# Optimization experiments

Measured on AMD Instinct MI355X. Metric: run time of the kernel, lower is better.

Reference implementation:

```python
import jax, jax.numpy as jnp
import numpy as np

N, E, NFEAT, H = 100000, 1600000, 128, 128
NLAYER = 3


def setup_inputs() -> dict:
    key = jax.random.key(0)
    ks = jax.random.split(key, 20)
    s = 0.05
    return {
        "features": jax.random.normal(ks[0], (N, NFEAT), jnp.float32),
        "edge_index": jax.random.randint(ks[1], (2, E), 0, N, jnp.int32),
        "edge_weight": jax.random.uniform(ks[2], (E,), jnp.float32),
        "w1": jax.random.normal(ks[3], (H, NFEAT), jnp.float32) * s,
        "b1": jnp.zeros((H,), jnp.float32),
        "gin_w1": jax.random.normal(ks[4], (NLAYER, H, H), jnp.float32) * s,
        "gin_b1": jnp.zeros((NLAYER, H), jnp.float32),
        "gin_w2": jax.random.normal(ks[5], (NLAYER, H, H), jnp.float32) * s,
        "gin_b2": jnp.zeros((NLAYER, H), jnp.float32),
        "gru_wih": jax.random.normal(ks[6], (NLAYER, 3 * H, H), jnp.float32) * s,
        "gru_whh": jax.random.normal(ks[7], (NLAYER, 3 * H, H), jnp.float32) * s,
        "gru_bih": jnp.zeros((NLAYER, 3 * H), jnp.float32),
        "gru_bhh": jnp.zeros((NLAYER, 3 * H), jnp.float32),
        "head_w1": jax.random.normal(ks[8], (NLAYER, H, H), jnp.float32) * s,
        "head_b1": jnp.zeros((NLAYER, H), jnp.float32),
        "head_w2_0": jax.random.normal(ks[9], (2, H), jnp.float32) * s,
        "head_b2_0": jnp.zeros((2,), jnp.float32),
        "head_w2_1": jax.random.normal(ks[10], (6, H), jnp.float32) * s,
        "head_b2_1": jnp.zeros((6,), jnp.float32),
        "head_w2_2": jax.random.normal(ks[11], (21, H), jnp.float32) * s,
        "head_b2_2": jnp.zeros((21,), jnp.float32),
    }


def _gru_cell(x, h, wih, whh, bih, bhh):
    # torch.nn.GRUCell semantics
    gi = x @ wih.T + bih           # [N, 3H]
    gh = h @ whh.T + bhh           # [N, 3H]
    ir, iz, inn = jnp.split(gi, 3, axis=1)
    hr, hz, hn = jnp.split(gh, 3, axis=1)
    r = jax.nn.sigmoid(ir + hr)
    z = jax.nn.sigmoid(iz + hz)
    n = jnp.tanh(inn + r * hn)
    return (1.0 - z) * n + z * h


def reference(features, edge_index, edge_weight, w1, b1,
              gin_w1, gin_b1, gin_w2, gin_b2,
              gru_wih, gru_whh, gru_bih, gru_bhh,
              head_w1, head_b1,
              head_w2_0, head_b2_0, head_w2_1, head_b2_1, head_w2_2, head_b2_2):
    n_nodes = features.shape[0]
    dst, src = edge_index[0], edge_index[1]  # spmm: out[dst] += w * x[src]
    head_w2 = [head_w2_0, head_w2_1, head_w2_2]
    head_b2 = [head_b2_0, head_b2_1, head_b2_2]

    x = jax.nn.relu(features @ w1.T + b1)  # mlp1 + ReLU
    layer_info = x
    outputs, _outputs = [], []
    for i in range(NLAYER):
        agg = jax.ops.segment_sum(edge_weight[:, None] * x[src], dst,
                                  num_segments=n_nodes)
        h = _gru_cell(agg, layer_info, gru_wih[i], gru_whh[i],
                      gru_bih[i], gru_bhh[i])
        # GinMlp: Linear -> ReLU -> Linear, then outer ReLU
        x = jax.nn.relu(h @ gin_w1[i].T + gin_b1[i]) @ gin_w2[i].T + gin_b2[i]
        x = jax.nn.relu(x)
        # custom layer-norm variant
        x = x / jnp.sqrt(1.0 + jnp.sum(x * x, axis=1, keepdims=True))
        # prediction head for this layer (mlpPos = [0,1,2])
        tmp = jax.nn.relu(x @ head_w1[i].T + head_b1[i]) @ head_w2[i].T + head_b2[i]
        outputs.append(jax.nn.log_softmax(tmp, axis=1))
        _outputs.append(jax.nn.softmax(tmp, axis=1))
        layer_info = x
    return tuple(outputs) + tuple(_outputs)
```

## Files before the change

### kernel.cpp

```cpp
#include <hip/hip_runtime.h>
#include <cstdint>
#include <cstddef>


typedef short  v8s __attribute__((ext_vector_type(8)));
typedef float  v4f __attribute__((ext_vector_type(4)));

static __device__ __forceinline__ float bf2f(uint16_t u) {
  return __uint_as_float(((uint32_t)u) << 16);
}
static __device__ __forceinline__ uint16_t f2b(float f) {
  uint32_t x = __float_as_uint(f);
  return (uint16_t)((x + 0x7FFFu + ((x >> 16) & 1u)) >> 16);
}
static __device__ __forceinline__ float sigmoidf_(float v) {
  return 1.f / (1.f + __expf(-v));
}

__global__ void k_detect(const uint32_t* __restrict__ u, int* __restrict__ flag) {
  int lane = threadIdx.x;
  uint32_t low = u[lane] & 0xFFFFu;
  uint32_t e = (low >> 7) & 0xFFu;
  bool pass = (e == 0) || (e >= 110 && e <= 141);
  unsigned long long b = __ballot(pass);
  if (lane == 0) *flag = (__popcll(b) >= 32) ? 1 : 0;
}

struct CvtDesc {
  const void* src[18];
  int off[19];
};

__global__ void k_cvtw(CvtDesc c, float* __restrict__ wbase,
                       uint16_t* __restrict__ wb16,
                       const int* __restrict__ flag, int total) {
  int gid = blockIdx.x * 256 + threadIdx.x;
  if (gid >= total) return;
  int t = 0;
#pragma unroll
  for (int i = 1; i < 18; i++)
    if (gid >= c.off[i]) t = i;
  int local = gid - c.off[t];
  float v;
  if (*flag) v = bf2f(((const uint16_t*)c.src[t])[local]);
  else       v = ((const float*)c.src[t])[local];
  wbase[gid] = v;
  wb16[gid] = f2b(v);
}

__global__ void k_cvt_feat(const void* __restrict__ src, uint16_t* __restrict__ dst,
                           int n, const int* __restrict__ flag) {
  int i = blockIdx.x * 256 + threadIdx.x;
  if (i >= n) return;
  if (*flag) dst[i] = ((const uint16_t*)src)[i];
  else       dst[i] = f2b(((const float*)src)[i]);
}

__global__ void k_zero_i(int* __restrict__ p, int n) {
  int i = blockIdx.x * 256 + threadIdx.x;
  if (i < n) p[i] = 0;
}

__global__ void k_zero_f(float* __restrict__ p, int n) {
  int i = blockIdx.x * 256 + threadIdx.x;
  if (i < n) p[i] = 0.f;
}

__global__ void k_pack_mm(const uint16_t* __restrict__ src, uint16_t* __restrict__ dst,
                          int nmat) {
  int id = blockIdx.x * 256 + threadIdx.x;
  if (id >= nmat * 2048) return;
  int mat = id >> 11;
  int rem = id & 2047;
  int blk = rem >> 6, lane = rem & 63;
  int kc = blk >> 3, t = blk & 7;
  int n0 = lane & 15, quad = lane >> 4;
  const uint16_t* s = src + (size_t)mat * 16384 + (size_t)(t * 16 + n0) * 128 + kc * 32 + quad * 8;
  uint16_t* d = dst + (size_t)id * 8;
  *reinterpret_cast<v8s*>(d) = *reinterpret_cast<const v8s*>(s);
}

__global__ void k_pack_gru(const uint16_t* __restrict__ wih, const uint16_t* __restrict__ whh,
                           uint16_t* __restrict__ dst, int nlayer) {
  int id = blockIdx.x * 256 + threadIdx.x;
  if (id >= nlayer * 192 * 64) return;
  int lane = id & 63;
  int blk = (id >> 6) % 192;
  int layer = (id >> 6) / 192;
  int g = blk % 3;
  int mat = (blk / 3) % 2;
  int u = (blk / 6) % 2;
  int w = (blk / 12) % 4;
  int kc = blk / 48;
  int n0 = lane & 15, quad = lane >> 4;
  const uint16_t* base = (mat == 0 ? wih : whh) + (size_t)layer * 384 * 128;
  const uint16_t* s = base + (size_t)(g * 128 + w * 32 + u * 16 + n0) * 128 + kc * 32 + quad * 8;
  uint16_t* d = dst + ((size_t)layer * 192 + blk) * 512 + (size_t)lane * 8;
  *reinterpret_cast<v8s*>(d) = *reinterpret_cast<const v8s*>(s);
}

__global__ void k_hist(const int* __restrict__ dst, int* __restrict__ deg2, int E) {
  int e = blockIdx.x * 256 + threadIdx.x;
  if (e < E) atomicAdd(&deg2[(size_t)dst[e] * 8 + (blockIdx.x & 7)], 1);
}

__global__ void k_scan1(const int* __restrict__ deg, int* __restrict__ bsum, int n) {
  __shared__ int red[256];
  int t = threadIdx.x;
  int base = blockIdx.x * 1024;
  int s = 0;
#pragma unroll
  for (int i = 0; i < 4; i++) {
    int idx = base + i * 256 + t;
    if (idx < n) s += deg[idx];
  }
  red[t] = s;
  __syncthreads();
  for (int off = 128; off > 0; off >>= 1) {
    if (t < off) red[t] += red[t + off];
    __syncthreads();
  }
  if (t == 0) bsum[blockIdx.x] = red[0];
}

__global__ void k_scan2(int* bsum, int nb, int* rowptr, int n) {
  __shared__ int red[256];
  int t = threadIdx.x;
  int v[4];
  int s = 0;
#pragma unroll
  for (int i = 0; i < 4; i++) {
    int idx = t * 4 + i;
    v[i] = (idx < nb) ? bsum[idx] : 0;
    s += v[i];
  }
  red[t] = s;
  __syncthreads();
  for (int off = 1; off < 256; off <<= 1) {
    int u = (t >= off) ? red[t - off] : 0;
    __syncthreads();
    red[t] += u;
    __syncthreads();
  }
  int run = red[t] - s;
#pragma unroll
  for (int i = 0; i < 4; i++) {
    int idx = t * 4 + i;
    if (idx < nb) { bsum[idx] = run; run += v[i]; }
  }
  if (t == 255) rowptr[n] = red[255];
}

__global__ void k_scan3(const int* __restrict__ deg, const int* __restrict__ bsum,
                        int* __restrict__ rowptr, int* __restrict__ cursor, int n) {
  __shared__ int lds[256];
  int t = threadIdx.x;
  int base = blockIdx.x * 1024 + t * 4;
  int v0 = 0, v1 = 0, v2 = 0, v3 = 0;
  if (base + 0 < n) v0 = deg[base + 0];
  if (base + 1 < n) v1 = deg[base + 1];
  if (base + 2 < n) v2 = deg[base + 2];
  if (base + 3 < n) v3 = deg[base + 3];
  int s = v0 + v1 + v2 + v3;
  lds[t] = s;
  __syncthreads();
  for (int off = 1; off < 256; off <<= 1) {
    int u = (t >= off) ? lds[t - off] : 0;
    __syncthreads();
    lds[t] += u;
    __syncthreads();
  }
  int run = lds[t] - s + bsum[blockIdx.x];
  if (base + 0 < n) { rowptr[base + 0] = run; cursor[base + 0] = run; run += v0; }
  if (base + 1 < n) { rowptr[base + 1] = run; cursor[base + 1] = run; run += v1; }
  if (base + 2 < n) { rowptr[base + 2] = run; cursor[base + 2] = run; run += v2; }
  if (base + 3 < n) { rowptr[base + 3] = run; cursor[base + 3] = run; run += v3; }
}

__global__ void k_scatter(const int* __restrict__ dst, const int* __restrict__ src,
                          const void* __restrict__ w, int* __restrict__ cursor2,
                          uint2* __restrict__ ep, const int* __restrict__ flag, int E) {
  int e = blockIdx.x * 256 + threadIdx.x;
  if (e < E) {
    int d = dst[e];
    int pos = atomicAdd(&cursor2[(size_t)d * 8 + (blockIdx.x & 7)], 1);
    float wv;
    if (*flag) wv = bf2f(((const uint16_t*)w)[e]);
    else       wv = ((const float*)w)[e];
    ep[pos] = make_uint2((uint32_t)src[e], __float_as_uint(wv));
  }
}

__global__ void k_spmm(const uint16_t* __restrict__ x, const int* __restrict__ rowptr2,
                       const uint2* __restrict__ ep, uint16_t* __restrict__ agg, int n) {
  int node = blockIdx.x * 4 + (threadIdx.x >> 6);
  int lane = threadIdx.x & 63;
  if (node >= n) return;
  int p0 = rowptr2[(size_t)node * 8], p1 = rowptr2[(size_t)node * 8 + 8];
  float a0 = 0.f, a1 = 0.f;
  int p = p0;
  for (; p + 3 < p1; p += 4) {
    uint2 e0 = ep[p], e1 = ep[p + 1], e2 = ep[p + 2], e3 = ep[p + 3];
    uint32_t u0 = *reinterpret_cast<const uint32_t*>(x + (size_t)e0.x * 128 + lane * 2);
    uint32_t u1 = *reinterpret_cast<const uint32_t*>(x + (size_t)e1.x * 128 + lane * 2);
    uint32_t u2 = *reinterpret_cast<const uint32_t*>(x + (size_t)e2.x * 128 + lane * 2);
    uint32_t u3 = *reinterpret_cast<const uint32_t*>(x + (size_t)e3.x * 128 + lane * 2);
    float w0 = __uint_as_float(e0.y), w1 = __uint_as_float(e1.y);
    float w2 = __uint_as_float(e2.y), w3 = __uint_as_float(e3.y);
    a0 = fmaf(w0, bf2f((uint16_t)u0), a0);
    a1 = fmaf(w0, bf2f((uint16_t)(u0 >> 16)), a1);
    a0 = fmaf(w1, bf2f((uint16_t)u1), a0);
    a1 = fmaf(w1, bf2f((uint16_t)(u1 >> 16)), a1);
    a0 = fmaf(w2, bf2f((uint16_t)u2), a0);
    a1 = fmaf(w2, bf2f((uint16_t)(u2 >> 16)), a1);
    a0 = fmaf(w3, bf2f((uint16_t)u3), a0);
    a1 = fmaf(w3, bf2f((uint16_t)(u3 >> 16)), a1);
  }
  for (; p < p1; p++) {
    uint2 e0 = ep[p];
    float w0 = __uint_as_float(e0.y);
    uint32_t u0 = *reinterpret_cast<const uint32_t*>(x + (size_t)e0.x * 128 + lane * 2);
    a0 = fmaf(w0, bf2f((uint16_t)u0), a0);
    a1 = fmaf(w0, bf2f((uint16_t)(u0 >> 16)), a1);
  }
  uint32_t packed = (uint32_t)f2b(a0) | ((uint32_t)f2b(a1) << 16);
  *reinterpret_cast<uint32_t*>(agg + (size_t)node * 128 + lane * 2) = packed;
}

template <int EPI>
__launch_bounds__(256)
__global__ void k_mm(const uint16_t* __restrict__ A, const uint16_t* __restrict__ Wrp,
                     const float* __restrict__ bias, uint16_t* __restrict__ C,
                     int nrows) {
  int wave = threadIdx.x >> 6, lane = threadIdx.x & 63;
  int n0 = lane & 15, quad = lane >> 4;
  int m0 = (blockIdx.x * 4 + wave) * 32;
  int r0 = m0 + n0, r1 = m0 + 16 + n0;
  bool ok0 = r0 < nrows, ok1 = r1 < nrows;
  const v8s z8 = {0, 0, 0, 0, 0, 0, 0, 0};

  v4f acc[2][8];
#pragma unroll
  for (int rt = 0; rt < 2; rt++)
#pragma unroll
    for (int t = 0; t < 8; t++) acc[rt][t] = {0.f, 0.f, 0.f, 0.f};

  const uint16_t* ap0 = A + (size_t)r0 * 128 + quad * 8;
  const uint16_t* ap1 = A + (size_t)r1 * 128 + quad * 8;
#pragma unroll
  for (int kc = 0; kc < 4; kc++) {
    v8s a0 = ok0 ? *reinterpret_cast<const v8s*>(ap0 + kc * 32) : z8;
    v8s a1 = ok1 ? *reinterpret_cast<const v8s*>(ap1 + kc * 32) : z8;
    const uint16_t* wp = Wrp + (size_t)kc * 4096 + (size_t)lane * 8;
#pragma unroll
    for (int t = 0; t < 8; t++) {
      v8s bf = *reinterpret_cast<const v8s*>(wp + t * 512);
      acc[0][t] = __builtin_amdgcn_mfma_f32_16x16x32_bf16(a0, bf, acc[0][t], 0, 0, 0);
      acc[1][t] = __builtin_amdgcn_mfma_f32_16x16x32_bf16(a1, bf, acc[1][t], 0, 0, 0);
    }
  }

#pragma unroll
  for (int rt = 0; rt < 2; rt++) {
    int mb = m0 + rt * 16;
    float vv[8][4];
#pragma unroll
    for (int t = 0; t < 8; t++) {
      float b = bias[t * 16 + n0];
#pragma unroll
      for (int r = 0; r < 4; r++) vv[t][r] = fmaxf(acc[rt][t][r] + b, 0.f);
    }
    if (EPI == 2) {
#pragma unroll
      for (int r = 0; r < 4; r++) {
        float ss = 0.f;
#pragma unroll
        for (int t = 0; t < 8; t++) ss = fmaf(vv[t][r], vv[t][r], ss);
        ss += __shfl_xor(ss, 1);
        ss += __shfl_xor(ss, 2);
        ss += __shfl_xor(ss, 4);
        ss += __shfl_xor(ss, 8);
        float sc = rsqrtf(1.f + ss);
#pragma unroll
        for (int t = 0; t < 8; t++) vv[t][r] *= sc;
      }
    }
#pragma unroll
    for (int r = 0; r < 4; r++) {
      int row = mb + quad * 4 + r;
      if (row >= nrows) continue;
#pragma unroll
      for (int t = 0; t < 8; t++)
        C[(size_t)row * 128 + t * 16 + n0] = f2b(vv[t][r]);
    }
  }
}

template <int C>
__launch_bounds__(256)
__global__ void k_mmh(const uint16_t* __restrict__ A, const uint16_t* __restrict__ Wrp,
                      const float* __restrict__ bias,
                      const float* __restrict__ w2, const float* __restrict__ b2,
                      float* __restrict__ out_log, float* __restrict__ out_soft,
                      int nrows) {
  __shared__ uint16_t hl[128][130];
  int wave = threadIdx.x >> 6, lane = threadIdx.x & 63;
  int n0 = lane & 15, quad = lane >> 4;
  int m0 = (blockIdx.x * 4 + wave) * 32;
  int r0 = m0 + n0, r1 = m0 + 16 + n0;
  bool ok0 = r0 < nrows, ok1 = r1 < nrows;
  const v8s z8 = {0, 0, 0, 0, 0, 0, 0, 0};

  v4f acc[2][8];
#pragma unroll
  for (int rt = 0; rt < 2; rt++)
#pragma unroll
    for (int t = 0; t < 8; t++) acc[rt][t] = {0.f, 0.f, 0.f, 0.f};

  const uint16_t* ap0 = A + (size_t)r0 * 128 + quad * 8;
  const uint16_t* ap1 = A + (size_t)r1 * 128 + quad * 8;
#pragma unroll
  for (int kc = 0; kc < 4; kc++) {
    v8s a0 = ok0 ? *reinterpret_cast<const v8s*>(ap0 + kc * 32) : z8;
    v8s a1 = ok1 ? *reinterpret_cast<const v8s*>(ap1 + kc * 32) : z8;
    const uint16_t* wp = Wrp + (size_t)kc * 4096 + (size_t)lane * 8;
#pragma unroll
    for (int t = 0; t < 8; t++) {
      v8s bf = *reinterpret_cast<const v8s*>(wp + t * 512);
      acc[0][t] = __builtin_amdgcn_mfma_f32_16x16x32_bf16(a0, bf, acc[0][t], 0, 0, 0);
      acc[1][t] = __builtin_amdgcn_mfma_f32_16x16x32_bf16(a1, bf, acc[1][t], 0, 0, 0);
    }
  }

#pragma unroll
  for (int rt = 0; rt < 2; rt++) {
#pragma unroll
    for (int t = 0; t < 8; t++) {
      float b = bias[t * 16 + n0];
#pragma unroll
      for (int r = 0; r < 4; r++) {
        int rl = wave * 32 + rt * 16 + quad * 4 + r;
        hl[rl][t * 16 + n0] = f2b(fmaxf(acc[rt][t][r] + b, 0.f));
      }
    }
  }
  __syncthreads();

  int tid = threadIdx.x;
  if (tid < 128) {
    int node = blockIdx.x * 128 + tid;
    if (node < nrows) {
      float lg[C];
#pragma unroll
      for (int c = 0; c < C; c++) lg[c] = b2[c];
      for (int k = 0; k < 64; k++) {
        uint32_t u = *reinterpret_cast<const uint32_t*>(&hl[tid][2 * k]);
        float x0 = bf2f((uint16_t)u);
        float x1 = bf2f((uint16_t)(u >> 16));
#pragma unroll
        for (int c = 0; c < C; c++) lg[c] = fmaf(x0, w2[c * 128 + 2 * k], lg[c]);
#pragma unroll
        for (int c = 0; c < C; c++) lg[c] = fmaf(x1, w2[c * 128 + 2 * k + 1], lg[c]);
      }
      float m = lg[0];
#pragma unroll
      for (int c = 1; c < C; c++) m = fmaxf(m, lg[c]);
      float s = 0.f;
      float e[C];
#pragma unroll
      for (int c = 0; c < C; c++) { e[c] = __expf(lg[c] - m); s += e[c]; }
      float ls = __logf(s);
      float inv = 1.f / s;
#pragma unroll
      for (int c = 0; c < C; c++) {
        out_log[(size_t)node * C + c] = lg[c] - m - ls;
        out_soft[(size_t)node * C + c] = e[c] * inv;
      }
    }
  }
}

__launch_bounds__(256)
__global__ void k_grug(const uint16_t* aggio, const uint16_t* __restrict__ xb,
                       const uint16_t* __restrict__ Wrp,
                       const uint16_t* __restrict__ G1rp,
                       const float* __restrict__ bih, const float* __restrict__ bhh,
                       const float* __restrict__ gb1,
                       uint16_t* hidout, int n) {
  __shared__ uint16_t hl[32][136];
  int wave = threadIdx.x >> 6, lane = threadIdx.x & 63;
  int n0 = lane & 15, quad = lane >> 4;
  int m0 = blockIdx.x * 32;
  int r0 = m0 + n0, r1 = m0 + 16 + n0;
  bool ok0 = r0 < n, ok1 = r1 < n;
  const v8s z8 = {0, 0, 0, 0, 0, 0, 0, 0};

  v4f accI[2][2][3], accH[2][2][3];
#pragma unroll
  for (int rt = 0; rt < 2; rt++)
#pragma unroll
    for (int u = 0; u < 2; u++)
#pragma unroll
      for (int g = 0; g < 3; g++) {
        accI[rt][u][g] = {0.f, 0.f, 0.f, 0.f};
        accH[rt][u][g] = {0.f, 0.f, 0.f, 0.f};
      }

  const uint16_t* ap0 = aggio + (size_t)r0 * 128 + quad * 8;
  const uint16_t* ap1 = aggio + (size_t)r1 * 128 + quad * 8;
  const uint16_t* xp0 = xb + (size_t)r0 * 128 + quad * 8;
  const uint16_t* xp1 = xb + (size_t)r1 * 128 + quad * 8;
#pragma unroll
  for (int kc = 0; kc < 4; kc++) {
    v8s a0 = ok0 ? *reinterpret_cast<const v8s*>(ap0 + kc * 32) : z8;
    v8s a1 = ok1 ? *reinterpret_cast<const v8s*>(ap1 + kc * 32) : z8;
    v8s x0 = ok0 ? *reinterpret_cast<const v8s*>(xp0 + kc * 32) : z8;
    v8s x1 = ok1 ? *reinterpret_cast<const v8s*>(xp1 + kc * 32) : z8;
    const uint16_t* wp = Wrp + (size_t)((kc * 4 + wave) * 12) * 512 + (size_t)lane * 8;
#pragma unroll
    for (int u = 0; u < 2; u++) {
#pragma unroll
      for (int g = 0; g < 3; g++) {
        v8s bi = *reinterpret_cast<const v8s*>(wp + (u * 6 + g) * 512);
        v8s bh = *reinterpret_cast<const v8s*>(wp + (u * 6 + 3 + g) * 512);
        accI[0][u][g] = __builtin_amdgcn_mfma_f32_16x16x32_bf16(a0, bi, accI[0][u][g], 0, 0, 0);
        accI[1][u][g] = __builtin_amdgcn_mfma_f32_16x16x32_bf16(a1, bi, accI[1][u][g], 0, 0, 0);
        accH[0][u][g] = __builtin_amdgcn_mfma_f32_16x16x32_bf16(x0, bh, accH[0][u][g], 0, 0, 0);
        accH[1][u][g] = __builtin_amdgcn_mfma_f32_16x16x32_bf16(x1, bh, accH[1][u][g], 0, 0, 0);
      }
    }
  }

#pragma unroll
  for (int rt = 0; rt < 2; rt++) {
#pragma unroll
    for (int u = 0; u < 2; u++) {
      int col = wave * 32 + u * 16 + n0;
      float bir = bih[col], biz = bih[128 + col], bin = bih[256 + col];
      float bhr = bhh[col], bhz = bhh[128 + col], bhn = bhh[256 + col];
#pragma unroll
      for (int r = 0; r < 4; r++) {
        int rl = rt * 16 + quad * 4 + r;
        int row = m0 + rl;
        float ir = accI[rt][u][0][r] + bir;
        float iz = accI[rt][u][1][r] + biz;
        float in_ = accI[rt][u][2][r] + bin;
        float hr = accH[rt][u][0][r] + bhr;
        float hz = accH[rt][u][1][r] + bhz;
        float hn = accH[rt][u][2][r] + bhn;
        float rr = sigmoidf_(ir + hr);
        float zz = sigmoidf_(iz + hz);
        float nn = tanhf(fmaf(rr, hn, in_));
        float xv = (row < n) ? bf2f(xb[(size_t)row * 128 + col]) : 0.f;
        hl[rl][col] = f2b(fmaf(zz, xv - nn, nn));
      }
    }
  }
  __syncthreads();

  v4f acc2[2][2];
#pragma unroll
  for (int rt = 0; rt < 2; rt++)
#pragma unroll
    for (int u = 0; u < 2; u++) acc2[rt][u] = {0.f, 0.f, 0.f, 0.f};

#pragma unroll
  for (int kc = 0; kc < 4; kc++) {
    v8s a0 = *reinterpret_cast<const v8s*>(&hl[n0][kc * 32 + quad * 8]);
    v8s a1 = *reinterpret_cast<const v8s*>(&hl[16 + n0][kc * 32 + quad * 8]);
#pragma unroll
    for (int u = 0; u < 2; u++) {
      int t = wave * 2 + u;
      v8s bf = *reinterpret_cast<const v8s*>(G1rp + (size_t)kc * 4096 + (size_t)t * 512 + (size_t)lane * 8);
      acc2[0][u] = __builtin_amdgcn_mfma_f32_16x16x32_bf16(a0, bf, acc2[0][u], 0, 0, 0);
      acc2[1][u] = __builtin_amdgcn_mfma_f32_16x16x32_bf16(a1, bf, acc2[1][u], 0, 0, 0);
    }
  }

#pragma unroll
  for (int rt = 0; rt < 2; rt++) {
#pragma unroll
    for (int u = 0; u < 2; u++) {
      int col = wave * 32 + u * 16 + n0;
      float b = gb1[col];
#pragma unroll
      for (int r = 0; r < 4; r++) {
        int row = m0 + rt * 16 + quad * 4 + r;
        if (row < n)
          hidout[(size_t)row * 128 + col] = f2b(fmaxf(acc2[rt][u][r] + b, 0.f));
      }
    }
  }
}

extern "C" void kernel_launch(void* const* d_in, const int* in_sizes, int n_in,
                              void* d_out, int out_size, void* d_ws, size_t ws_size,
                              hipStream_t stream) {
  const int N = in_sizes[0] / 128;
  const int E = in_sizes[2];
  const int N8 = N * 8;

  static const int wn[18] = {16384, 128, 49152, 384, 49152, 384,
                             147456, 147456, 1152, 1152, 49152, 384,
                             256, 2, 768, 6, 2688, 21};
  CvtDesc cd;
  int off = 0;
  for (int i = 0; i < 18; i++) {
    cd.src[i] = d_in[3 + i];
    cd.off[i] = off;
    off += wn[i];
  }
  cd.off[18] = off;
  const int wtotal = off;

  char* p = (char*)d_ws;
  size_t used = 0;
  auto alloc = [&](size_t bytes) -> char* {
    char* r = p;
    size_t b = (bytes + 255) & ~(size_t)255;
    p += b;
    used += b;
    return r;
  };
  int*      flag    = (int*)alloc(256);
  float*    wbase   = (float*)alloc((size_t)wtotal * 4);
  uint16_t* wb16    = (uint16_t*)alloc((size_t)wtotal * 2);
  uint16_t* mmrp    = (uint16_t*)alloc((size_t)10 * 16384 * 2);
  uint16_t* grurp   = (uint16_t*)alloc((size_t)3 * 192 * 512 * 2);
  uint16_t* xb      = (uint16_t*)alloc((size_t)N * 128 * 2);
  uint16_t* aggb    = (uint16_t*)alloc((size_t)N * 128 * 2);
  int*      deg2    = (int*)alloc((size_t)N8 * 4);
  int*      rowptr2 = (int*)alloc((size_t)(N8 + 1) * 4);
  int*      cursor2 = (int*)alloc((size_t)N8 * 4);
  uint2*    epack   = (uint2*)alloc((size_t)E * 8);
  int*      bsum    = (int*)alloc(4096);

  float* out = (float*)d_out;
  float* outlog[3]  = {out, out + 2 * (size_t)N, out + 8 * (size_t)N};
  float* outsoft[3] = {out + 29 * (size_t)N, out + 31 * (size_t)N, out + 37 * (size_t)N};

  if (used > ws_size) {
    k_zero_f<<<(out_size + 255) / 256, 256, 0, stream>>>(out, out_size);
    return;
  }

  float* b1f   = wbase + cd.off[1];
  float* ginb1 = wbase + cd.off[3];
  float* ginb2 = wbase + cd.off[5];
  float* bih   = wbase + cd.off[8];
  float* bhh   = wbase + cd.off[9];
  float* hb1   = wbase + cd.off[11];
  float* hw2_0 = wbase + cd.off[12];
  float* hb2_0 = wbase + cd.off[13];
  float* hw2_1 = wbase + cd.off[14];
  float* hb2_1 = wbase + cd.off[15];
  float* hw2_2 = wbase + cd.off[16];
  float* hb2_2 = wbase + cd.off[17];

  uint16_t* w1b   = wb16 + cd.off[0];
  uint16_t* ginw1b= wb16 + cd.off[2];
  uint16_t* ginw2b= wb16 + cd.off[4];
  uint16_t* wihb  = wb16 + cd.off[6];
  uint16_t* whhb  = wb16 + cd.off[7];
  uint16_t* hw1b  = wb16 + cd.off[10];

  uint16_t* w1rp    = mmrp;
  uint16_t* ginw1rp = mmrp + (size_t)1 * 16384;
  uint16_t* ginw2rp = mmrp + (size_t)4 * 16384;
  uint16_t* hw1rp   = mmrp + (size_t)7 * 16384;

  const int* dst = (const int*)d_in[1];
  const int* src = (const int*)d_in[1] + E;

  k_detect<<<1, 64, 0, stream>>>((const uint32_t*)d_in[0], flag);
  k_cvtw<<<(wtotal + 255) / 256, 256, 0, stream>>>(cd, wbase, wb16, flag, wtotal);
  k_cvt_feat<<<((size_t)N * 128 + 255) / 256, 256, 0, stream>>>(d_in[0], aggb,
                                                                N * 128, flag);
  k_pack_mm<<<(1 * 2048 + 255) / 256, 256, 0, stream>>>(w1b, w1rp, 1);
  k_pack_mm<<<(3 * 2048 + 255) / 256, 256, 0, stream>>>(ginw1b, ginw1rp, 3);
  k_pack_mm<<<(3 * 2048 + 255) / 256, 256, 0, stream>>>(ginw2b, ginw2rp, 3);
  k_pack_mm<<<(3 * 2048 + 255) / 256, 256, 0, stream>>>(hw1b, hw1rp, 3);
  k_pack_gru<<<(3 * 192 * 64 + 255) / 256, 256, 0, stream>>>(wihb, whhb, grurp, 3);

  k_zero_i<<<(N8 + 255) / 256, 256, 0, stream>>>(deg2, N8);
  k_hist<<<(E + 255) / 256, 256, 0, stream>>>(dst, deg2, E);
  int nb = (N8 + 1023) / 1024;
  k_scan1<<<nb, 256, 0, stream>>>(deg2, bsum, N8);
  k_scan2<<<1, 256, 0, stream>>>(bsum, nb, rowptr2, N8);
  k_scan3<<<nb, 256, 0, stream>>>(deg2, bsum, rowptr2, cursor2, N8);
  k_scatter<<<(E + 255) / 256, 256, 0, stream>>>(dst, src, d_in[2], cursor2,
                                                 epack, flag, E);

  int mmrb = (N + 127) / 128;
  int grub = (N + 31) / 32;
  int spb  = (N + 3) / 4;

  k_mm<1><<<mmrb, 256, 0, stream>>>(aggb, w1rp, b1f, xb, N);

  for (int i = 0; i < 3; i++) {
    k_spmm<<<spb, 256, 0, stream>>>(xb, rowptr2, epack, aggb, N);
    k_grug<<<grub, 256, 0, stream>>>(aggb, xb, grurp + (size_t)i * 192 * 512,
                                     ginw1rp + (size_t)i * 16384,
                                     bih + i * 384, bhh + i * 384,
                                     ginb1 + i * 128, aggb, N);
    k_mm<2><<<mmrb, 256, 0, stream>>>(aggb, ginw2rp + (size_t)i * 16384,
                                      ginb2 + i * 128, xb, N);
    if (i == 0)
      k_mmh<2><<<mmrb, 256, 0, stream>>>(xb, hw1rp, hb1, hw2_0, hb2_0,
                                         outlog[0], outsoft[0], N);
    else if (i == 1)
      k_mmh<6><<<mmrb, 256, 0, stream>>>(xb, hw1rp + (size_t)16384, hb1 + 128,
                                         hw2_1, hb2_1, outlog[1], outsoft[1], N);
    else
      k_mmh<21><<<mmrb, 256, 0, stream>>>(xb, hw1rp + (size_t)2 * 16384, hb1 + 256,
                                          hw2_2, hb2_2, outlog[2], outsoft[2], N);
  }
}
```

Measured before the change: 1.017 ms.

## Rebuild CSR with two-level bucketed scatter and split GRU into persistent LDS-weight kernel

The CSR build now bins edges by 128-node buckets with a per-bucket cursor, then places them within each bucket using LDS atomics. This replaces the old 8-way-striped per-node cursors and gives a plain CSR rowptr for the SpMM. The fused GRU+GIN-first-linear kernel is split: a persistent GRU kernel keeps its column slice of the gate weights in LDS and loops over row tiles, and the GIN first linear runs through the existing k_mm<1> path. This adds an extra N×128 bf16 round trip and another edge-sized buffer in exchange for weight reuse and cheaper atomics. It also swaps in a fast exp-based tanh.

After: 1.099 ms. +8.1%, slower.

```diff
diff --git a/kernel.cpp b/kernel.cpp
--- a/kernel.cpp
+++ b/kernel.cpp
@@ -15,6 +15,9 @@
 }
 static __device__ __forceinline__ float sigmoidf_(float v) {
   return 1.f / (1.f + __expf(-v));
+}
+static __device__ __forceinline__ float tanhf_(float v) {
+  return 1.f - 2.f / (__expf(2.f * v) + 1.f);
 }
 
 __global__ void k_detect(const uint32_t* __restrict__ u, int* __restrict__ flag) {
@@ -99,9 +102,14 @@
   *reinterpret_cast<v8s*>(d) = *reinterpret_cast<const v8s*>(s);
 }
 
-__global__ void k_hist(const int* __restrict__ dst, int* __restrict__ deg2, int E) {
+__global__ void k_hist2(const int* __restrict__ dst, int* __restrict__ deg,
+                        int* __restrict__ bdeg, int E) {
   int e = blockIdx.x * 256 + threadIdx.x;
-  if (e < E) atomicAdd(&deg2[(size_t)dst[e] * 8 + (blockIdx.x & 7)], 1);
+  if (e < E) {
+    int d = dst[e];
+    atomicAdd(&deg[d], 1);
+    atomicAdd(&bdeg[(d >> 7) * 8 + (blockIdx.x & 7)], 1);
+  }
 }
 
 __global__ void k_scan1(const int* __restrict__ deg, int* __restrict__ bsum, int n) {
@@ -152,7 +160,7 @@
 }
 
 __global__ void k_scan3(const int* __restrict__ deg, const int* __restrict__ bsum,
-                        int* __restrict__ rowptr, int* __restrict__ cursor, int n) {
+                        int* __restrict__ rowptr, int n) {
   __shared__ int lds[256];
   int t = threadIdx.x;
   int base = blockIdx.x * 1024 + t * 4;
@@ -171,32 +179,81 @@
     __syncthreads();
   }
   int run = lds[t] - s + bsum[blockIdx.x];
-  if (base + 0 < n) { rowptr[base + 0] = run; cursor[base + 0] = run; run += v0; }
-  if (base + 1 < n) { rowptr[base + 1] = run; cursor[base + 1] = run; run += v1; }
-  if (base + 2 < n) { rowptr[base + 2] = run; cursor[base + 2] = run; run += v2; }
-  if (base + 3 < n) { rowptr[base + 3] = run; cursor[base + 3] = run; run += v3; }
-}
-
-__global__ void k_scatter(const int* __restrict__ dst, const int* __restrict__ src,
-                          const void* __restrict__ w, int* __restrict__ cursor2,
-                          uint2* __restrict__ ep, const int* __restrict__ flag, int E) {
+  if (base + 0 < n) { rowptr[base + 0] = run; run += v0; }
+  if (base + 1 < n) { rowptr[base + 1] = run; run += v1; }
+  if (base + 2 < n) { rowptr[base + 2] = run; run += v2; }
+  if (base + 3 < n) { rowptr[base + 3] = run; run += v3; }
+}
+
+__global__ void k_bscan(const int* __restrict__ bdeg, int* __restrict__ bptr,
+                        int* __restrict__ bcur, int total) {
+  __shared__ int red[256];
+  int t = threadIdx.x;
+  int chunk = (total + 255) >> 8;
+  int beg = t * chunk;
+  int end = beg + chunk;
+  if (end > total) end = total;
+  int s = 0;
+  for (int i = beg; i < end; i++) s += bdeg[i];
+  red[t] = s;
+  __syncthreads();
+  for (int off = 1; off < 256; off <<= 1) {
+    int u = (t >= off) ? red[t - off] : 0;
+    __syncthreads();
+    red[t] += u;
+    __syncthreads();
+  }
+  int run = red[t] - s;
+  for (int i = beg; i < end; i++) {
+    int v = bdeg[i];
+    bptr[i] = run;
+    bcur[i] = run;
+    run += v;
+  }
+  if (t == 255) bptr[total] = red[255];
+}
+
+__global__ void k_scatter1(const int* __restrict__ dst, const int* __restrict__ src,
+                           const void* __restrict__ w, int* __restrict__ bcur,
+                           uint2* __restrict__ ep0, const int* __restrict__ flag, int E) {
   int e = blockIdx.x * 256 + threadIdx.x;
   if (e < E) {
     int d = dst[e];
-    int pos = atomicAdd(&cursor2[(size_t)d * 8 + (blockIdx.x & 7)], 1);
+    int pos = atomicAdd(&bcur[(d >> 7) * 8 + (blockIdx.x & 7)], 1);
     float wv;
     if (*flag) wv = bf2f(((const uint16_t*)w)[e]);
     else       wv = ((const float*)w)[e];
-    ep[pos] = make_uint2((uint32_t)src[e], __float_as_uint(wv));
-  }
-}
-
-__global__ void k_spmm(const uint16_t* __restrict__ x, const int* __restrict__ rowptr2,
+    ep0[pos] = make_uint2((uint32_t)src[e] | (((uint32_t)d & 127u) << 25),
+                          __float_as_uint(wv));
+  }
+}
+
+__global__ void k_scatter2(const uint2* __restrict__ ep0, const int* __restrict__ bptr,
+                           const int* __restrict__ rowptr, uint2* __restrict__ ep,
+                           int n) {
+  __shared__ int lcur[128];
+  int b = blockIdx.x;
+  int t = threadIdx.x;
+  if (t < 128) {
+    int nd = (b << 7) + t;
+    lcur[t] = (nd < n) ? rowptr[nd] : 0;
+  }
+  __syncthreads();
+  int p0 = bptr[b * 8], p1 = bptr[b * 8 + 8];
+  for (int p = p0 + t; p < p1; p += 256) {
+    uint2 v = ep0[p];
+    int dl = v.x >> 25;
+    int pos = atomicAdd(&lcur[dl], 1);
+    ep[pos] = make_uint2(v.x & 0x01FFFFFFu, v.y);
+  }
+}
+
+__global__ void k_spmm(const uint16_t* __restrict__ x, const int* __restrict__ rowptr,
                        const uint2* __restrict__ ep, uint16_t* __restrict__ agg, int n) {
   int node = blockIdx.x * 4 + (threadIdx.x >> 6);
   int lane = threadIdx.x & 63;
   if (node >= n) return;
-  int p0 = rowptr2[(size_t)node * 8], p1 = rowptr2[(size_t)node * 8 + 8];
+  int p0 = rowptr[node], p1 = rowptr[node + 1];
   float a0 = 0.f, a1 = 0.f;
   int p = p0;
   for (; p + 3 < p1; p += 4) {
@@ -296,6 +353,102 @@
   }
 }
 
+__launch_bounds__(256)
+__global__ void k_gru(const uint16_t* __restrict__ agg, const uint16_t* __restrict__ xb,
+                      const uint16_t* __restrict__ Wrp,
+                      const float* __restrict__ bih, const float* __restrict__ bhh,
+                      uint16_t* __restrict__ hb, int n, int ntiles, int nrb) {
+  __shared__ uint16_t wl[48][512];
+  int s = blockIdx.x & 3;
+  int rb = blockIdx.x >> 2;
+  int wave = threadIdx.x >> 6, lane = threadIdx.x & 63;
+  int n0 = lane & 15, quad = lane >> 4;
+  const v8s z8 = {0, 0, 0, 0, 0, 0, 0, 0};
+
+  for (int c = threadIdx.x; c < 3072; c += 256) {
+    int f = c >> 6;
+    int w8 = (c & 63) << 3;
+    int kc = f / 12, j = f % 12;
+    const uint16_t* g = Wrp + (size_t)((kc * 4 + s) * 12 + j) * 512 + w8;
+    *reinterpret_cast<v8s*>(&wl[f][w8]) = *reinterpret_cast<const v8s*>(g);
+  }
+  __syncthreads();
+
+  float bi_r[2], bi_z[2], bi_n[2], bh_r[2], bh_z[2], bh_n[2];
+#pragma unroll
+  for (int u = 0; u < 2; u++) {
+    int col = s * 32 + u * 16 + n0;
+    bi_r[u] = bih[col]; bi_z[u] = bih[128 + col]; bi_n[u] = bih[256 + col];
+    bh_r[u] = bhh[col]; bh_z[u] = bhh[128 + col]; bh_n[u] = bhh[256 + col];
+  }
+
+  for (int t = rb; t < ntiles; t += nrb) {
+    int m0 = t * 128 + wave * 32;
+    int r0 = m0 + n0, r1 = m0 + 16 + n0;
+    bool ok0 = r0 < n, ok1 = r1 < n;
+
+    v4f accI[2][2][3], accH[2][2][3];
+#pragma unroll
+    for (int rt = 0; rt < 2; rt++)
+#pragma unroll
+      for (int u = 0; u < 2; u++)
+#pragma unroll
+        for (int g = 0; g < 3; g++) {
+          accI[rt][u][g] = {0.f, 0.f, 0.f, 0.f};
+          accH[rt][u][g] = {0.f, 0.f, 0.f, 0.f};
+        }
+
+    const uint16_t* ap0 = agg + (size_t)r0 * 128 + quad * 8;
+    const uint16_t* ap1 = agg + (size_t)r1 * 128 + quad * 8;
+    const uint16_t* xp0 = xb + (size_t)r0 * 128 + quad * 8;
+    const uint16_t* xp1 = xb + (size_t)r1 * 128 + quad * 8;
+#pragma unroll
+    for (int kc = 0; kc < 4; kc++) {
+      v8s a0 = ok0 ? *reinterpret_cast<const v8s*>(ap0 + kc * 32) : z8;
+      v8s a1 = ok1 ? *reinterpret_cast<const v8s*>(ap1 + kc * 32) : z8;
+      v8s x0 = ok0 ? *reinterpret_cast<const v8s*>(xp0 + kc * 32) : z8;
+      v8s x1 = ok1 ? *reinterpret_cast<const v8s*>(xp1 + kc * 32) : z8;
+#pragma unroll
+      for (int u = 0; u < 2; u++) {
+#pragma unroll
+        for (int g = 0; g < 3; g++) {
+          v8s bi = *reinterpret_cast<const v8s*>(&wl[kc * 12 + u * 6 + g][(size_t)lane * 8]);
+          v8s bh = *reinterpret_cast<const v8s*>(&wl[kc * 12 + u * 6 + 3 + g][(size_t)lane * 8]);
+          accI[0][u][g] = __builtin_amdgcn_mfma_f32_16x16x32_bf16(a0, bi, accI[0][u][g], 0, 0, 0);
+          accI[1][u][g] = __builtin_amdgcn_mfma_f32_16x16x32_bf16(a1, bi, accI[1][u][g], 0, 0, 0);
+          accH[0][u][g] = __builtin_amdgcn_mfma_f32_16x16x32_bf16(x0, bh, accH[0][u][g], 0, 0, 0);
+          accH[1][u][g] = __builtin_amdgcn_mfma_f32_16x16x32_bf16(x1, bh, accH[1][u][g], 0, 0, 0);
+        }
+      }
+    }
+
+#pragma unroll
+    for (int rt = 0; rt < 2; rt++) {
+#pragma unroll
+      for (int u = 0; u < 2; u++) {
+        int col = s * 32 + u * 16 + n0;
+#pragma unroll
+        for (int r = 0; r < 4; r++) {
+          int row = m0 + rt * 16 + quad * 4 + r;
+          if (row < n) {
+            float ir = accI[rt][u][0][r] + bi_r[u];
+            float iz = accI[rt][u][1][r] + bi_z[u];
+            float in_ = accI[rt][u][2][r] + bi_n[u];
+            float hr = accH[rt][u][0][r] + bh_r[u];
+            float hz = accH[rt][u][1][r] + bh_z[u];
+            float hn = accH[rt][u][2][r] + bh_n[u];
+            float rr = sigmoidf_(ir + hr);
+            float zz = sigmoidf_(iz + hz);
+            float nn = tanhf_(fmaf(rr, hn, in_));
+            float xv = bf2f(xb[(size_t)row * 128 + col]);
+            hb[(size_t)row * 128 + col] = f2b(fmaf(zz, xv - nn, nn));
+          }
+        }
+      }
+    }
+  }
+}
+
 template <int C>
 __launch_bounds__(256)
 __global__ void k_mmh(const uint16_t* __restrict__ A, const uint16_t* __restrict__ Wrp,
@@ -365,129 +518,16 @@
       float m = lg[0];
 #pragma unroll
       for (int c = 1; c < C; c++) m = fmaxf(m, lg[c]);
-      float s = 0.f;
+      float sum = 0.f;
       float e[C];
 #pragma unroll
-      for (int c = 0; c < C; c++) { e[c] = __expf(lg[c] - m); s += e[c]; }
-      float ls = __logf(s);
-      float inv = 1.f / s;
+      for (int c = 0; c < C; c++) { e[c] = __expf(lg[c] - m); sum += e[c]; }
+      float ls = __logf(sum);
+      float inv = 1.f / sum;
 #pragma unroll
       for (int c = 0; c < C; c++) {
         out_log[(size_t)node * C + c] = lg[c] - m - ls;
         out_soft[(size_t)node * C + c] = e[c] * inv;
-      }
-    }
-  }
-}
-
-__launch_bounds__(256)
-__global__ void k_grug(const uint16_t* aggio, const uint16_t* __restrict__ xb,
-                       const uint16_t* __restrict__ Wrp,
-                       const uint16_t* __restrict__ G1rp,
-                       const float* __restrict__ bih, const float* __restrict__ bhh,
-                       const float* __restrict__ gb1,
-                       uint16_t* hidout, int n) {
-  __shared__ uint16_t hl[32][136];
-  int wave = threadIdx.x >> 6, lane = threadIdx.x & 63;
-  int n0 = lane & 15, quad = lane >> 4;
-  int m0 = blockIdx.x * 32;
-  int r0 = m0 + n0, r1 = m0 + 16 + n0;
-  bool ok0 = r0 < n, ok1 = r1 < n;
-  const v8s z8 = {0, 0, 0, 0, 0, 0, 0, 0};
-
-  v4f accI[2][2][3], accH[2][2][3];
-#pragma unroll
-  for (int rt = 0; rt < 2; rt++)
-#pragma unroll
-    for (int u = 0; u < 2; u++)
-#pragma unroll
-      for (int g = 0; g < 3; g++) {
-        accI[rt][u][g] = {0.f, 0.f, 0.f, 0.f};
-        accH[rt][u][g] = {0.f, 0.f, 0.f, 0.f};
-      }
-
-  const uint16_t* ap0 = aggio + (size_t)r0 * 128 + quad * 8;
-  const uint16_t* ap1 = aggio + (size_t)r1 * 128 + quad * 8;
-  const uint16_t* xp0 = xb + (size_t)r0 * 128 + quad * 8;
-  const uint16_t* xp1 = xb + (size_t)r1 * 128 + quad * 8;
-#pragma unroll
-  for (int kc = 0; kc < 4; kc++) {
-    v8s a0 = ok0 ? *reinterpret_cast<const v8s*>(ap0 + kc * 32) : z8;
-    v8s a1 = ok1 ? *reinterpret_cast<const v8s*>(ap1 + kc * 32) : z8;
-    v8s x0 = ok0 ? *reinterpret_cast<const v8s*>(xp0 + kc * 32) : z8;
-    v8s x1 = ok1 ? *reinterpret_cast<const v8s*>(xp1 + kc * 32) : z8;
-    const uint16_t* wp = Wrp + (size_t)((kc * 4 + wave) * 12) * 512 + (size_t)lane * 8;
-#pragma unroll
-    for (int u = 0; u < 2; u++) {
-#pragma unroll
-      for (int g = 0; g < 3; g++) {
-        v8s bi = *reinterpret_cast<const v8s*>(wp + (u * 6 + g) * 512);
-        v8s bh = *reinterpret_cast<const v8s*>(wp + (u * 6 + 3 + g) * 512);
-        accI[0][u][g] = __builtin_amdgcn_mfma_f32_16x16x32_bf16(a0, bi, accI[0][u][g], 0, 0, 0);
-        accI[1][u][g] = __builtin_amdgcn_mfma_f32_16x16x32_bf16(a1, bi, accI[1][u][g], 0, 0, 0);
-        accH[0][u][g] = __builtin_amdgcn_mfma_f32_16x16x32_bf16(x0, bh, accH[0][u][g], 0, 0, 0);
-        accH[1][u][g] = __builtin_amdgcn_mfma_f32_16x16x32_bf16(x1, bh, accH[1][u][g], 0, 0, 0);
-      }
-    }
-  }
-
-#pragma unroll
-  for (int rt = 0; rt < 2; rt++) {
-#pragma unroll
-    for (int u = 0; u < 2; u++) {
-      int col = wave * 32 + u * 16 + n0;
-      float bir = bih[col], biz = bih[128 + col], bin = bih[256 + col];
-      float bhr = bhh[col], bhz = bhh[128 + col], bhn = bhh[256 + col];
-#pragma unroll
-      for (int r = 0; r < 4; r++) {
-        int rl = rt * 16 + quad * 4 + r;
-        int row = m0 + rl;
-        float ir = accI[rt][u][0][r] + bir;
-        float iz = accI[rt][u][1][r] + biz;
-        float in_ = accI[rt][u][2][r] + bin;
-        float hr = accH[rt][u][0][r] + bhr;
-        float hz = accH[rt][u][1][r] + bhz;
-        float hn = accH[rt][u][2][r] + bhn;
-        float rr = sigmoidf_(ir + hr);
-        float zz = sigmoidf_(iz + hz);
-        float nn = tanhf(fmaf(rr, hn, in_));
-        float xv = (row < n) ? bf2f(xb[(size_t)row * 128 + col]) : 0.f;
-        hl[rl][col] = f2b(fmaf(zz, xv - nn, nn));
-      }
-    }
-  }
-  __syncthreads();
-
-  v4f acc2[2][2];
-#pragma unroll
-  for (int rt = 0; rt < 2; rt++)
-#pragma unroll
-    for (int u = 0; u < 2; u++) acc2[rt][u] = {0.f, 0.f, 0.f, 0.f};
-
-#pragma unroll
-  for (int kc = 0; kc < 4; kc++) {
-    v8s a0 = *reinterpret_cast<const v8s*>(&hl[n0][kc * 32 + quad * 8]);
-    v8s a1 = *reinterpret_cast<const v8s*>(&hl[16 + n0][kc * 32 + quad * 8]);
-#pragma unroll
-    for (int u = 0; u < 2; u++) {
-      int t = wave * 2 + u;
-      v8s bf = *reinterpret_cast<const v8s*>(G1rp + (size_t)kc * 4096 + (size_t)t * 512 + (size_t)lane * 8);
-      acc2[0][u] = __builtin_amdgcn_mfma_f32_16x16x32_bf16(a0, bf, acc2[0][u], 0, 0, 0);
-      acc2[1][u] = __builtin_amdgcn_mfma_f32_16x16x32_bf16(a1, bf, acc2[1][u], 0, 0, 0);
-    }
-  }
-
-#pragma unroll
-  for (int rt = 0; rt < 2; rt++) {
-#pragma unroll
-    for (int u = 0; u < 2; u++) {
-      int col = wave * 32 + u * 16 + n0;
-      float b = gb1[col];
-#pragma unroll
-      for (int r = 0; r < 4; r++) {
-        int row = m0 + rt * 16 + quad * 4 + r;
-        if (row < n)
-          hidout[(size_t)row * 128 + col] = f2b(fmaxf(acc2[rt][u][r] + b, 0.f));
       }
     }
   }
@@ -498,7 +538,8 @@
                               hipStream_t stream) {
   const int N = in_sizes[0] / 128;
   const int E = in_sizes[2];
-  const int N8 = N * 8;
+  const int NB = (N + 127) >> 7;
+  const int NB8 = NB * 8;
 
   static const int wn[18] = {16384, 128, 49152, 384, 49152, 384,
                              147456, 147456, 1152, 1152, 49152, 384,
@@ -529,9 +570,13 @@
   uint16_t* grurp   = (uint16_t*)alloc((size_t)3 * 192 * 512 * 2);
   uint16_t* xb      = (uint16_t*)alloc((size_t)N * 128 * 2);
   uint16_t* aggb    = (uint16_t*)alloc((size_t)N * 128 * 2);
-  int*      deg2    = (int*)alloc((size_t)N8 * 4);
-  int*      rowptr2 = (int*)alloc((size_t)(N8 + 1) * 4);
-  int*      cursor2 = (int*)alloc((size_t)N8 * 4);
+  uint16_t* hb      = (uint16_t*)alloc((size_t)N * 128 * 2);
+  int*      deg     = (int*)alloc((size_t)N * 4);
+  int*      rowptr  = (int*)alloc((size_t)(N + 1) * 4);
+  int*      bdeg    = (int*)alloc((size_t)NB8 * 4);
+  int*      bptr    = (int*)alloc((size_t)(NB8 + 1) * 4);
+  int*      bcur    = (int*)alloc((size_t)NB8 * 4);
+  uint2*    ep0     = (uint2*)alloc((size_t)E * 8);
   uint2*    epack   = (uint2*)alloc((size_t)E * 8);
   int*      bsum    = (int*)alloc(4096);
 
@@ -582,27 +627,32 @@
   k_pack_mm<<<(3 * 2048 + 255) / 256, 256, 0, stream>>>(hw1b, hw1rp, 3);
   k_pack_gru<<<(3 * 192 * 64 + 255) / 256, 256, 0, stream>>>(wihb, whhb, grurp, 3);
 
-  k_zero_i<<<(N8 + 255) / 256, 256, 0, stream>>>(deg2, N8);
-  k_hist<<<(E + 255) / 256, 256, 0, stream>>>(dst, deg2, E);
-  int nb = (N8 + 1023) / 1024;
-  k_scan1<<<nb, 256, 0, stream>>>(deg2, bsum, N8);
-  k_scan2<<<1, 256, 0, stream>>>(bsum, nb, rowptr2, N8);
-  k_scan3<<<nb, 256, 0, stream>>>(deg2, bsum, rowptr2, cursor2, N8);
-  k_scatter<<<(E + 255) / 256, 256, 0, stream>>>(dst, src, d_in[2], cursor2,
-                                                 epack, flag, E);
+  k_zero_i<<<(N + 255) / 256, 256, 0, stream>>>(deg, N);
+  k_zero_i<<<(NB8 + 255) / 256, 256, 0, stream>>>(bdeg, NB8);
+  k_hist2<<<(E + 255) / 256, 256, 0, stream>>>(dst, deg, bdeg, E);
+  int nb = (N + 1023) / 1024;
+  k_scan1<<<nb, 256, 0, stream>>>(deg, bsum, N);
+  k_scan2<<<1, 256, 0, stream>>>(bsum, nb, rowptr, N);
+  k_scan3<<<nb, 256, 0, stream>>>(deg, bsum, rowptr, N);
+  k_bscan<<<1, 256, 0, stream>>>(bdeg, bptr, bcur, NB8);
+  k_scatter1<<<(E + 255) / 256, 256, 0, stream>>>(dst, src, d_in[2], bcur,
+                                                  ep0, flag, E);
+  k_scatter2<<<NB, 256, 0, stream>>>(ep0, bptr, rowptr, epack, N);
 
   int mmrb = (N + 127) / 128;
-  int grub = (N + 31) / 32;
   int spb  = (N + 3) / 4;
+  int ntiles = (N + 127) / 128;
+  const int NRB = 192;
 
   k_mm<1><<<mmrb, 256, 0, stream>>>(aggb, w1rp, b1f, xb, N);
 
   for (int i = 0; i < 3; i++) {
-    k_spmm<<<spb, 256, 0, stream>>>(xb, rowptr2, epack, aggb, N);
-    k_grug<<<grub, 256, 0, stream>>>(aggb, xb, grurp + (size_t)i * 192 * 512,
-                                     ginw1rp + (size_t)i * 16384,
-                                     bih + i * 384, bhh + i * 384,
-                                     ginb1 + i * 128, aggb, N);
+    k_spmm<<<spb, 256, 0, stream>>>(xb, rowptr, epack, aggb, N);
+    k_gru<<<4 * NRB, 256, 0, stream>>>(aggb, xb, grurp + (size_t)i * 192 * 512,
+                                       bih + i * 384, bhh + i * 384, hb, N,
+                                       ntiles, NRB);
+    k_mm<1><<<mmrb, 256, 0, stream>>>(hb, ginw1rp + (size_t)i * 16384,
+                                      ginb1 + i * 128, aggb, N);
     k_mm<2><<<mmrb, 256, 0, stream>>>(aggb, ginw2rp + (size_t)i * 16384,
                                       ginb2 + i * 128, xb, N);
     if (i == 0)
```
